# Kernel tuning notes

Hardware: AMD Instinct MI355X
Metric: run time of the kernel (lower is better)

Reference implementation:

```python
import jax, jax.numpy as jnp
import numpy as np

N = 50000   # nodes
E = 800000  # edges
IN = 128    # in_channels
H = 256     # hidden_channels
G = 128     # graphs in batch
NEG_SLOPE = 0.2


def _gat_conv(x, src, dst, W, a_src, a_dst, b):
    # PyG GATConv, heads=1: xp = W x; e_ij = LeakyReLU(a_src.xp_j + a_dst.xp_i);
    # softmax over incoming edges of target i; out_i = sum_j alpha_ij xp_j + b
    xp = x @ W                                   # [N, H]
    e = jax.nn.leaky_relu(xp[src] @ a_src + xp[dst] @ a_dst, NEG_SLOPE)  # [Et]
    m = jax.ops.segment_max(e, dst, num_segments=N)
    m = jnp.where(jnp.isfinite(m), m, 0.0)
    p = jnp.exp(e - m[dst])
    denom = jax.ops.segment_sum(p, dst, num_segments=N)
    alpha = p / denom[dst]
    return jax.ops.segment_sum(alpha[:, None] * xp[src], dst, num_segments=N) + b


def _gru_step_h0(x, W_ih, W_hh, b_ih, b_hh):
    # torch.nn.GRU, seq_len=1, h0=0. Gate order: r, z, n.
    gi = x @ W_ih.T + b_ih                       # [N, 3H]
    i_r, i_z, i_n = jnp.split(gi, 3, axis=-1)
    h_r, h_z, h_n = jnp.split(b_hh, 3)           # h0=0 -> hidden gates are biases
    r = jax.nn.sigmoid(i_r + h_r)
    z = jax.nn.sigmoid(i_z + h_z)
    n = jnp.tanh(i_n + r * h_n)
    return (1.0 - z) * n                         # + z * h0 (=0)


def setup_inputs() -> dict:
    key = jax.random.key(0)
    ks = jax.random.split(key, 18)
    s = 0.05
    inp = {
        "x": jax.random.normal(ks[0], (N, IN), jnp.float32),
        "edge_index": jax.random.randint(ks[1], (2, E), 0, N, dtype=jnp.int32).astype(jnp.int64),
        "batch": jnp.sort(jax.random.randint(ks[2], (N,), 0, G, dtype=jnp.int32)).astype(jnp.int64),
        # GAT layer 0 (in->H) and layer 1 (H->H)
        "W0": jax.random.normal(ks[3], (IN, H), jnp.float32) * s,
        "a_src0": jax.random.normal(ks[4], (H,), jnp.float32) * s,
        "a_dst0": jax.random.normal(ks[5], (H,), jnp.float32) * s,
        "b0": jnp.zeros((H,), jnp.float32),
        "W1": jax.random.normal(ks[6], (H, H), jnp.float32) * s,
        "a_src1": jax.random.normal(ks[7], (H,), jnp.float32) * s,
        "a_dst1": jax.random.normal(ks[8], (H,), jnp.float32) * s,
        "b1": jnp.zeros((H,), jnp.float32),
        # GRU(H, H)
        "W_ih": jax.random.normal(ks[9], (3 * H, H), jnp.float32) * s,
        "W_hh": jax.random.normal(ks[10], (3 * H, H), jnp.float32) * s,
        "b_ih": jnp.zeros((3 * H,), jnp.float32),
        "b_hh": jnp.zeros((3 * H,), jnp.float32),
        # super_node_fc
        "Wf": jax.random.normal(ks[11], (H, H), jnp.float32) * s,
        "bf": jnp.zeros((H,), jnp.float32),
    }
    return inp


def reference(x, edge_index, batch, W0, a_src0, a_dst0, b0, W1, a_src1, a_dst1, b1,
              W_ih, W_hh, b_ih, b_hh, Wf, bf):
    # add self loops (PyG GATConv default)
    loops = jnp.arange(N, dtype=edge_index.dtype)
    src = jnp.concatenate([edge_index[0], loops])
    dst = jnp.concatenate([edge_index[1], loops])

    h = jax.nn.relu(_gat_conv(x, src, dst, W0, a_src0, a_dst0, b0))  # dropout=identity (eval)
    h = jax.nn.relu(_gat_conv(h, src, dst, W1, a_src1, a_dst1, b1))

    h = _gru_step_h0(h, W_ih, W_hh, b_ih, b_hh)                      # [N, H]

    h = jax.ops.segment_sum(h, batch, num_segments=G)                # global_add_pool [G, H]
    super_node = jnp.mean(h, axis=0, keepdims=True)                  # [1, H]
    super_node = jax.nn.relu(super_node @ Wf.T + bf)
    return jnp.concatenate([h, jnp.broadcast_to(super_node, (G, H))], axis=1)  # [G, 2H]
```

## Files before the change

### kernel.cpp

```cpp
#include <hip/hip_runtime.h>
#include <hip/hip_fp16.h>
#include <math.h>

#define N_NODES 50000
#define N_PAD   50176
#define N_EDGES 800000
#define ET (N_EDGES + N_NODES)
#define IN_CH 128
#define H 256
#define G_GRAPHS 128
#define NEG_SLOPE 0.2f
#define GRU_CHUNK 25000
#define NB 391

typedef __attribute__((ext_vector_type(8))) short short8;
typedef __attribute__((ext_vector_type(4))) float f32x4;
typedef unsigned short u16;
typedef unsigned char u8;

#if __has_builtin(__builtin_amdgcn_cvt_f32_fp8) && __has_builtin(__builtin_amdgcn_cvt_pk_fp8_f32)
#define USE_FP8_BUILTINS 1
#else
#define USE_FP8_BUILTINS 0
#endif

__device__ inline u16 f2bf(float v) {
    unsigned u = __float_as_uint(v);
    unsigned r = (u + 0x7FFFu + ((u >> 16) & 1u)) >> 16;
    return (u16)r;
}
__device__ inline float bf2f(u16 v) {
    return __uint_as_float(((unsigned)v) << 16);
}

#if USE_FP8_BUILTINS
#define FP8_WSCALE 1.0f
__device__ inline unsigned fp8_pack4(float a, float b, float c, float d) {
    int v = 0;
    v = __builtin_amdgcn_cvt_pk_fp8_f32(a, b, v, false);
    v = __builtin_amdgcn_cvt_pk_fp8_f32(c, d, v, true);
    return (unsigned)v;
}
__device__ inline void fp8_dec4(unsigned rv, float& f0, float& f1, float& f2, float& f3) {
    f0 = __builtin_amdgcn_cvt_f32_fp8((int)rv, 0);
    f1 = __builtin_amdgcn_cvt_f32_fp8((int)rv, 1);
    f2 = __builtin_amdgcn_cvt_f32_fp8((int)rv, 2);
    f3 = __builtin_amdgcn_cvt_f32_fp8((int)rv, 3);
}
#else
#define FP8_WSCALE 256.0f
__device__ inline u8 fp8_enc1(float f) {
    unsigned u = __float_as_uint(f);
    unsigned s = (u >> 31) << 7;
    float a = fabsf(f);
    if (a >= 448.f) return (u8)(s | 0x7E);
    unsigned bits = __float_as_uint(a);
    int exp = (int)((bits >> 23) & 255) - 127;
    unsigned m23 = bits & 0x7fffff;
    if (exp < -6) {
        int m = (int)rintf(a * 512.f);
        if (m >= 8) return (u8)(s | (1 << 3));
        return (u8)(s | m);
    }
    int e8 = exp + 7;
    unsigned m = m23 >> 20, rem = m23 & 0xFFFFF;
    if (rem > 0x80000 || (rem == 0x80000 && (m & 1))) m++;
    if (m == 8) { m = 0; e8++; }
    if (e8 > 15 || (e8 == 15 && m == 7)) return (u8)(s | 0x7E);
    return (u8)(s | (e8 << 3) | m);
}
__device__ inline unsigned fp8_pack4(float a, float b, float c, float d) {
    return (unsigned)fp8_enc1(a) | ((unsigned)fp8_enc1(b) << 8) |
           ((unsigned)fp8_enc1(c) << 16) | ((unsigned)fp8_enc1(d) << 24);
}
__device__ inline void fp8_dec4(unsigned rv, float& f0, float& f1, float& f2, float& f3) {
    unsigned hA = ((rv & 0x00800080u) << 8) | ((rv & 0x007f007fu) << 7);
    unsigned rs = rv >> 8;
    unsigned hB = ((rs & 0x00800080u) << 8) | ((rs & 0x007f007fu) << 7);
    __half2 a = *(__half2*)&hA;
    __half2 b = *(__half2*)&hB;
    f0 = __low2float(a);  f2 = __high2float(a);
    f1 = __low2float(b);  f3 = __high2float(b);
}
#endif

__device__ inline void async_cp16(const u16* g, u16* l) {
    __builtin_amdgcn_global_load_lds(
        (const __attribute__((address_space(1))) unsigned int*)g,
        (__attribute__((address_space(3))) unsigned int*)l,
        16, 0, 0);
}


__global__ __launch_bounds__(256) void bucket_hist(const int* __restrict__ ei,
                                                   int* __restrict__ gcnt) {
    __shared__ int h[NB];
    int t = threadIdx.x;
    for (int b = t; b < NB; b += 256) h[b] = 0;
    __syncthreads();
    for (int e = blockIdx.x * 256 + t; e < N_EDGES; e += gridDim.x * 256)
        atomicAdd(&h[ei[N_EDGES + e] >> 7], 1);
    __syncthreads();
    for (int b = t; b < NB; b += 256)
        if (h[b]) atomicAdd(&gcnt[b], h[b]);
}

__global__ __launch_bounds__(512) void bucket_scan(const int* __restrict__ gcnt,
                                                   int* __restrict__ off,
                                                   int* __restrict__ cur) {
    __shared__ int s[NB + 1];
    int t = threadIdx.x;
    if (t < NB) s[t] = gcnt[t];
    __syncthreads();
    if (t == 0) {
        int a = 0;
        for (int b = 0; b < NB; b++) { int c = s[b]; s[b] = a; a += c; }
        s[NB] = a;
    }
    __syncthreads();
    if (t <= NB) { off[t] = s[t]; if (t < NB) cur[t] = s[t]; }
}

#define EPT 16
__global__ __launch_bounds__(256) void bucket_scatter(const int* __restrict__ ei,
                                                      int* __restrict__ bucketCur,
                                                      int2* __restrict__ rec) {
    __shared__ int cnt[NB];
    __shared__ int base[NB];
    int t = threadIdx.x;
    for (int b = t; b < NB; b += 256) cnt[b] = 0;
    __syncthreads();
    int e0 = blockIdx.x * (256 * EPT);
    int sa[EPT], da[EPT], rk[EPT];
#pragma unroll
    for (int k = 0; k < EPT; k++) {
        int e = e0 + k * 256 + t;
        if (e < N_EDGES) {
            sa[k] = ei[e];
            da[k] = ei[N_EDGES + e];
            rk[k] = atomicAdd(&cnt[da[k] >> 7], 1);
        }
    }
    __syncthreads();
    for (int b = t; b < NB; b += 256) {
        int c = cnt[b];
        base[b] = c ? atomicAdd(&bucketCur[b], c) : 0;
    }
    __syncthreads();
#pragma unroll
    for (int k = 0; k < EPT; k++) {
        int e = e0 + k * 256 + t;
        if (e < N_EDGES) rec[base[da[k] >> 7] + rk[k]] = make_int2(sa[k], da[k]);
    }
}

__global__ __launch_bounds__(256) void node_hist(const int2* __restrict__ rec,
                                                 const int* __restrict__ off,
                                                 int* __restrict__ counts) {
    __shared__ int cnt[128];
    int b = blockIdx.x, t = threadIdx.x;
    if (t < 128) cnt[t] = 1;
    __syncthreads();
    int lo = off[b], hi = off[b + 1];
    for (int i = lo + t; i < hi; i += 256) atomicAdd(&cnt[rec[i].y & 127], 1);
    __syncthreads();
    int node = b * 128 + t;
    if (t < 128 && node < N_NODES) counts[node] = cnt[t];
}

__global__ __launch_bounds__(256) void scan_block(const int* __restrict__ in,
                                                  int* __restrict__ incl,
                                                  int* __restrict__ blockSums) {
    __shared__ int s[256];
    int t = threadIdx.x;
    int i = blockIdx.x * 256 + t;
    int v = (i < N_NODES) ? in[i] : 0;
    s[t] = v;
    __syncthreads();
    for (int off = 1; off < 256; off <<= 1) {
        int x = 0;
        if (t >= off) x = s[t - off];
        __syncthreads();
        if (t >= off) s[t] += x;
        __syncthreads();
    }
    if (i < N_NODES) incl[i] = s[t];
    if (t == 255) blockSums[blockIdx.x] = s[255];
}

__global__ __launch_bounds__(256) void scan_sums(const int* __restrict__ blockSums,
                                                 int* __restrict__ blockOff, int nb) {
    __shared__ int s[256];
    int t = threadIdx.x;
    int v = (t < nb) ? blockSums[t] : 0;
    s[t] = v;
    __syncthreads();
    for (int off = 1; off < 256; off <<= 1) {
        int x = 0;
        if (t >= off) x = s[t - off];
        __syncthreads();
        if (t >= off) s[t] += x;
        __syncthreads();
    }
    if (t < nb) blockOff[t] = s[t] - v;
}

__global__ __launch_bounds__(256) void scan_finalize(const int* __restrict__ incl,
                                                     const int* __restrict__ blockOff,
                                                     int* __restrict__ indptr) {
    int i = blockIdx.x * 256 + threadIdx.x;
    if (i < N_NODES) indptr[i + 1] = incl[i] + blockOff[i >> 8];
    if (i == 0) indptr[0] = 0;
}

__global__ __launch_bounds__(256) void final_scatter(const int2* __restrict__ rec,
                                                     const int* __restrict__ off,
                                                     const int* __restrict__ indptr,
                                                     int* __restrict__ eidsSrc) {
    __shared__ int cur[128];
    int b = blockIdx.x, t = threadIdx.x;
    int node = b * 128 + t;
    if (t < 128 && node < N_NODES) {
        int ip = indptr[node];
        eidsSrc[ip] = node;
        cur[t] = ip + 1;
    }
    __syncthreads();
    int lo = off[b], hi = off[b + 1];
    for (int i = lo + t; i < hi; i += 256) {
        int2 r = rec[i];
        int pos = atomicAdd(&cur[r.y & 127], 1);
        eidsSrc[pos] = r.x;
    }
}

__global__ __launch_bounds__(256) void prep_kernel(const float* __restrict__ x,
                                                   const float* __restrict__ Wih,
                                                   const float* __restrict__ W0,
                                                   const float* __restrict__ W1,
                                                   u16* __restrict__ x_bf,
                                                   u16* __restrict__ Wih_bf,
                                                   u16* __restrict__ W0t,
                                                   u16* __restrict__ W1t) {
    int i = blockIdx.x * 256 + threadIdx.x;
    int seg = blockIdx.y;
    if (seg == 0) {
        if (i < N_NODES * IN_CH / 4) {
            float4 v = *(const float4*)&x[i * 4];
            ushort4 o = {f2bf(v.x), f2bf(v.y), f2bf(v.z), f2bf(v.w)};
            *(ushort4*)&x_bf[i * 4] = o;
        }
    } else if (seg == 1) {
        if (i < 3 * H * H / 4) {
            float4 v = *(const float4*)&Wih[i * 4];
            ushort4 o = {f2bf(v.x), f2bf(v.y), f2bf(v.z), f2bf(v.w)};
            *(ushort4*)&Wih_bf[i * 4] = o;
        }
    } else if (seg == 2) {
        if (i < IN_CH * H) {
            int k = i / H, n = i % H;
            W0t[(size_t)n * IN_CH + k] = f2bf(W0[i]);
        }
    } else {
        if (i < H * H) {
            int k = i / H, n = i % H;
            W1t[(size_t)n * H + k] = f2bf(W1[i]);
        }
    }
}

__global__ __launch_bounds__(256, 2) void gemm_wide(const u16* __restrict__ A,
                                                    const u16* __restrict__ Bt,
                                                    u16* __restrict__ C,
                                                    int M, int K, int Ntot) {
    __shared__ u16 As[128][32];
    __shared__ u16 Bs[256][32];
    int t = threadIdx.x;
    int m0 = blockIdx.x * 128;
    int n0 = blockIdx.y * 256;
    int wave = t >> 6, lane = t & 63;
    int wm = (wave >> 1) * 64, wn = (wave & 1) * 128;
    int lrow = lane & 15;
    int lq = lane >> 4;

    f32x4 acc[4][8];
#pragma unroll
    for (int i = 0; i < 4; i++)
#pragma unroll
        for (int j = 0; j < 8; j++)
            acc[i][j] = (f32x4){0.f, 0.f, 0.f, 0.f};

    int r0 = t >> 2, q0 = t & 3;
    const u16* gA0 = A + (size_t)(m0 + r0) * K + q0 * 8;
    const u16* gA1 = gA0 + (size_t)64 * K;
    const u16* gB0 = Bt + (size_t)(n0 + r0) * K + q0 * 8;
    const u16* gB1 = gB0 + (size_t)64 * K;
    const u16* gB2 = gB0 + (size_t)128 * K;
    const u16* gB3 = gB0 + (size_t)192 * K;
    u16* lA0 = &As[0][0] + t * 8;
    u16* lA1 = lA0 + 256 * 8;
    u16* lB0 = &Bs[0][0] + t * 8;
    u16* lB1 = lB0 + 256 * 8;
    u16* lB2 = lB0 + 512 * 8;
    u16* lB3 = lB0 + 768 * 8;

    for (int k0 = 0; k0 < K; k0 += 32) {
        __syncthreads();
        async_cp16(gA0 + k0, lA0);
        async_cp16(gA1 + k0, lA1);
        async_cp16(gB0 + k0, lB0);
        async_cp16(gB1 + k0, lB1);
        async_cp16(gB2 + k0, lB2);
        async_cp16(gB3 + k0, lB3);
        __syncthreads();
        short8 af[4], bfr[8];
#pragma unroll
        for (int i = 0; i < 4; i++)
            af[i] = *(const short8*)&As[wm + i * 16 + lrow][lq * 8];
#pragma unroll
        for (int j = 0; j < 8; j++)
            bfr[j] = *(const short8*)&Bs[wn + j * 16 + lrow][lq * 8];
#pragma unroll
        for (int i = 0; i < 4; i++)
#pragma unroll
            for (int j = 0; j < 8; j++)
                acc[i][j] = __builtin_amdgcn_mfma_f32_16x16x32_bf16(af[i], bfr[j], acc[i][j], 0, 0, 0);
    }
#pragma unroll
    for (int i = 0; i < 4; i++) {
#pragma unroll
        for (int reg = 0; reg < 4; reg++) {
            int gm = m0 + wm + i * 16 + lq * 4 + reg;
            if (gm < M) {
#pragma unroll
                for (int j = 0; j < 8; j++) {
                    int gn = n0 + wn + j * 16 + lrow;
                    C[(size_t)gm * Ntot + gn] = f2bf(acc[i][j][reg]);
                }
            }
        }
    }
}

__global__ __launch_bounds__(256) void sdot_fp8(const u16* __restrict__ xp,
                                                const float* __restrict__ a_src,
                                                const float* __restrict__ a_dst,
                                                float* __restrict__ s_src,
                                                float* __restrict__ s_dst,
                                                u8* __restrict__ xp8) {
    int wave = threadIdx.x >> 6, lane = threadIdx.x & 63;
    int n = blockIdx.x * 4 + wave;
    int col = lane << 2;
    ushort4 v = *(const ushort4*)&xp[(size_t)n * H + col];
    float4 a1 = *(const float4*)&a_src[col];
    float4 a2 = *(const float4*)&a_dst[col];
    float x0 = bf2f(v.x), x1 = bf2f(v.y), x2 = bf2f(v.z), x3 = bf2f(v.w);
    *(unsigned*)&xp8[(size_t)n * H + col] = fp8_pack4(x0, x1, x2, x3);
    float d1 = x0 * a1.x + x1 * a1.y + x2 * a1.z + x3 * a1.w;
    float d2 = x0 * a2.x + x1 * a2.y + x2 * a2.z + x3 * a2.w;
#pragma unroll
    for (int off = 32; off; off >>= 1) {
        d1 += __shfl_xor(d1, off);
        d2 += __shfl_xor(d2, off);
    }
    if (lane == 0) { s_src[n] = d1; s_dst[n] = d2; }
}

__global__ __launch_bounds__(256) void gat_agg_fp8(const u8* __restrict__ xp8,
                                                   const float* __restrict__ s_src,
                                                   const float* __restrict__ s_dst,
                                                   const int* __restrict__ indptr,
                                                   const int* __restrict__ eidsSrc,
                                                   const float* __restrict__ bias,
                                                   u16* __restrict__ out) {
    __shared__ int   sS[4][64];
    __shared__ float sW[4][64];
    int wave = threadIdx.x >> 6, lane = threadIdx.x & 63;
    int n = blockIdx.x * 4 + wave;
    int start = indptr[n];
    int deg = indptr[n + 1] - start;
    float sdn = s_dst[n];
    int col = lane << 2;
    float a0 = 0.f, a1 = 0.f, a2 = 0.f, a3 = 0.f;

    if (deg <= 64) {
        int s = 0;
        float v = -1e30f;
        if (lane < deg) {
            s = eidsSrc[start + lane];
            float u = s_src[s] + sdn;
            v = (u >= 0.f) ? u : NEG_SLOPE * u;
        }
        float m = v;
#pragma unroll
        for (int off = 32; off; off >>= 1) m = fmaxf(m, __shfl_xor(m, off));
        float pw = (lane < deg) ? expf(v - m) : 0.f;
        float dsum = pw;
#pragma unroll
        for (int off = 32; off; off >>= 1) dsum += __shfl_xor(dsum, off);
        sS[wave][lane] = s;
        sW[wave][lane] = pw * (FP8_WSCALE / dsum);
        int j = 0;
        for (; j + 8 <= deg; j += 8) {
            unsigned rv[8];
            float wv[8];
#pragma unroll
            for (int k = 0; k < 8; k++) {
                int sj = sS[wave][j + k];
                wv[k] = sW[wave][j + k];
                rv[k] = *(const unsigned*)&xp8[(size_t)sj * H + col];
            }
#pragma unroll
            for (int k = 0; k < 8; k++) {
                float f0, f1, f2, f3;
                fp8_dec4(rv[k], f0, f1, f2, f3);
                a0 += wv[k] * f0; a1 += wv[k] * f1;
                a2 += wv[k] * f2; a3 += wv[k] * f3;
            }
        }
        for (; j < deg; j++) {
            int sj = sS[wave][j];
            float wj = sW[wave][j];
            unsigned rv = *(const unsigned*)&xp8[(size_t)sj * H + col];
            float f0, f1, f2, f3;
            fp8_dec4(rv, f0, f1, f2, f3);
            a0 += wj * f0; a1 += wj * f1; a2 += wj * f2; a3 += wj * f3;
        }
    } else {
        float m = -1e30f;
        for (int i = lane; i < deg; i += 64) {
            int s = eidsSrc[start + i];
            float u = s_src[s] + sdn;
            u = (u >= 0.f) ? u : NEG_SLOPE * u;
            m = fmaxf(m, u);
        }
#pragma unroll
        for (int off = 32; off; off >>= 1) m = fmaxf(m, __shfl_xor(m, off));
        float dsum = 0.f;
        for (int i = lane; i < deg; i += 64) {
            int s = eidsSrc[start + i];
            float u = s_src[s] + sdn;
            u = (u >= 0.f) ? u : NEG_SLOPE * u;
            dsum += expf(u - m);
        }
#pragma unroll
        for (int off = 32; off; off >>= 1) dsum += __shfl_xor(dsum, off);
        float dinv = FP8_WSCALE / dsum;
        for (int base = 0; base < deg; base += 64) {
            int cnt = min(64, deg - base);
            int s = 0; float w = 0.f;
            if (lane < cnt) {
                s = eidsSrc[start + base + lane];
                float u = s_src[s] + sdn;
                u = (u >= 0.f) ? u : NEG_SLOPE * u;
                w = expf(u - m) * dinv;
            }
            sS[wave][lane] = s;
            sW[wave][lane] = w;
            for (int j = 0; j < cnt; j++) {
                int sj = sS[wave][j];
                float wj = sW[wave][j];
                unsigned rv = *(const unsigned*)&xp8[(size_t)sj * H + col];
                float f0, f1, f2, f3;
                fp8_dec4(rv, f0, f1, f2, f3);
                a0 += wj * f0; a1 += wj * f1; a2 += wj * f2; a3 += wj * f3;
            }
        }
    }
    float4 bv = *(const float4*)&bias[col];
    ushort4 o;
    o.x = f2bf(fmaxf(a0 + bv.x, 0.f));
    o.y = f2bf(fmaxf(a1 + bv.y, 0.f));
    o.z = f2bf(fmaxf(a2 + bv.z, 0.f));
    o.w = f2bf(fmaxf(a3 + bv.w, 0.f));
    *(ushort4*)&out[(size_t)n * H + col] = o;
}

__global__ __launch_bounds__(256) void gru_gates_pool(const u16* __restrict__ gates,
                                                      const float* __restrict__ b_ih,
                                                      const float* __restrict__ b_hh,
                                                      const int* __restrict__ batch,
                                                      float* __restrict__ pooled,
                                                      int nodeBase, int nodeCount) {
    int t = threadIdx.x;
    int i0 = blockIdx.x * 16;
    if (i0 >= nodeCount) return;
    float bir = b_ih[t], biz = b_ih[256 + t], bin_ = b_ih[512 + t];
    float bhr = b_hh[t], bhz = b_hh[256 + t], bhn = b_hh[512 + t];
    int iend = min(16, nodeCount - i0);
    float acc = 0.f;
    int cur_g = batch[nodeBase + i0];
    for (int i = 0; i < iend; i++) {
        size_t row = (size_t)(i0 + i) * 768;
        float ir = bf2f(gates[row + t]);
        float iz = bf2f(gates[row + 256 + t]);
        float in_ = bf2f(gates[row + 512 + t]);
        float r = 1.f / (1.f + expf(-(ir + bir + bhr)));
        float z = 1.f / (1.f + expf(-(iz + biz + bhz)));
        float nn = tanhf(in_ + bin_ + r * bhn);
        float h = (1.f - z) * nn;
        int g = batch[nodeBase + i0 + i];
        if (g != cur_g) {
            atomicAdd(&pooled[(size_t)cur_g * H + t], acc);
            acc = 0.f;
            cur_g = g;
        }
        acc += h;
    }
    atomicAdd(&pooled[(size_t)cur_g * H + t], acc);
}

__global__ __launch_bounds__(256) void super_kernel(const float* __restrict__ pooled,
                                                    const float* __restrict__ Wf,
                                                    const float* __restrict__ bf,
                                                    float* __restrict__ sup) {
    __shared__ float smean[256];
    int t = threadIdx.x;
    float s = 0.f;
    for (int g = 0; g < G_GRAPHS; g++) s += pooled[(size_t)g * H + t];
    smean[t] = s / (float)G_GRAPHS;
    __syncthreads();
    float acc = 0.f;
    for (int k = 0; k < H; k++) acc += smean[k] * Wf[(size_t)t * H + k];
    acc += bf[t];
    sup[t] = fmaxf(acc, 0.f);
}

__global__ __launch_bounds__(256) void writeout(const float* __restrict__ pooled,
                                                const float* __restrict__ sup,
                                                float* __restrict__ out) {
    int idx = blockIdx.x * 256 + threadIdx.x;
    int g = idx >> 9, c = idx & 511;
    out[idx] = (c < H) ? pooled[(size_t)g * H + c] : sup[c - H];
}

extern "C" void kernel_launch(void* const* d_in, const int* in_sizes, int n_in,
                              void* d_out, int out_size, void* d_ws, size_t ws_size,
                              hipStream_t stream) {
    const float* x      = (const float*)d_in[0];
    const int*   ei     = (const int*)d_in[1];
    const int*   batch  = (const int*)d_in[2];
    const float* W0     = (const float*)d_in[3];
    const float* a_src0 = (const float*)d_in[4];
    const float* a_dst0 = (const float*)d_in[5];
    const float* b0     = (const float*)d_in[6];
    const float* W1     = (const float*)d_in[7];
    const float* a_src1 = (const float*)d_in[8];
    const float* a_dst1 = (const float*)d_in[9];
    const float* b1     = (const float*)d_in[10];
    const float* W_ih   = (const float*)d_in[11];
    const float* b_ih   = (const float*)d_in[13];
    const float* b_hh   = (const float*)d_in[14];
    const float* Wf     = (const float*)d_in[15];
    const float* bf     = (const float*)d_in[16];
    float* out = (float*)d_out;

    char* p = (char*)d_ws;
    auto alloc = [&](size_t bytes) -> void* {
        void* r = (void*)p;
        p += (bytes + 255) & ~(size_t)255;
        return r;
    };
    u16*   xp_bf  = (u16*)alloc((size_t)N_PAD * H * 2);
    u16*   h_bf   = (u16*)alloc((size_t)N_PAD * H * 2);
    u16*   x_bf   = (u16*)alloc((size_t)N_PAD * IN_CH * 2);
    u8*    xp8    = (u8*)x_bf;
    u16*   gatesC = (u16*)alloc((size_t)GRU_CHUNK * 3 * H * 2);
    u16*   W0t    = (u16*)alloc((size_t)H * IN_CH * 2);
    u16*   W1t    = (u16*)alloc((size_t)H * H * 2);
    u16*   Wih_bf = (u16*)alloc((size_t)3 * H * H * 2);
    float* s_src  = (float*)alloc((size_t)N_NODES * 4);
    float* s_dst  = (float*)alloc((size_t)N_NODES * 4);
    int2*  rec    = (int2*)alloc((size_t)N_EDGES * 8);
    int*   eidsSrc= (int*)alloc((size_t)ET * 4);
    int*   counts = (int*)alloc((size_t)N_NODES * 4);
    int*   incl   = (int*)alloc((size_t)N_NODES * 4);
    int*   indptr = (int*)alloc((size_t)(N_NODES + 1) * 4);
    int*   gBkt   = (int*)alloc((size_t)(NB + 1) * 4);
    int*   bktOff = (int*)alloc((size_t)(NB + 1) * 4);
    int*   bktCur = (int*)alloc((size_t)(NB + 1) * 4);
    int*   bSums  = (int*)alloc(256 * 4);
    int*   bOff   = (int*)alloc(256 * 4);
    float* pooled = (float*)alloc((size_t)G_GRAPHS * H * 4);
    float* sup    = (float*)alloc((size_t)H * 4);

    const int SB = (N_NODES + 255) / 256;
    hipMemsetAsync(gBkt, 0, (size_t)NB * 4, stream);
    bucket_hist<<<NB, 256, 0, stream>>>(ei, gBkt);
    bucket_scan<<<1, 512, 0, stream>>>(gBkt, bktOff, bktCur);
    bucket_scatter<<<(N_EDGES + 256 * EPT - 1) / (256 * EPT), 256, 0, stream>>>(ei, bktCur, rec);
    node_hist<<<NB, 256, 0, stream>>>(rec, bktOff, counts);
    scan_block<<<SB, 256, 0, stream>>>(counts, incl, bSums);
    scan_sums<<<1, 256, 0, stream>>>(bSums, bOff, SB);
    scan_finalize<<<SB, 256, 0, stream>>>(incl, bOff, indptr);
    final_scatter<<<NB, 256, 0, stream>>>(rec, bktOff, indptr, eidsSrc);

    prep_kernel<<<dim3((N_NODES * IN_CH / 4 + 255) / 256, 4), 256, 0, stream>>>(
        x, W_ih, W0, W1, x_bf, Wih_bf, W0t, W1t);

    const int MB = (N_NODES + 127) / 128;
    const int WB = N_NODES / 4;
    gemm_wide<<<dim3(MB, 1), 256, 0, stream>>>(x_bf, W0t, xp_bf, N_NODES, IN_CH, H);
    sdot_fp8<<<WB, 256, 0, stream>>>(xp_bf, a_src0, a_dst0, s_src, s_dst, xp8);
    gat_agg_fp8<<<WB, 256, 0, stream>>>(xp8, s_src, s_dst, indptr, eidsSrc, b0, h_bf);
    gemm_wide<<<dim3(MB, 1), 256, 0, stream>>>(h_bf, W1t, xp_bf, N_NODES, H, H);
    sdot_fp8<<<WB, 256, 0, stream>>>(xp_bf, a_src1, a_dst1, s_src, s_dst, xp8);
    gat_agg_fp8<<<WB, 256, 0, stream>>>(xp8, s_src, s_dst, indptr, eidsSrc, b1, h_bf);
    hipMemsetAsync(pooled, 0, (size_t)G_GRAPHS * H * 4, stream);
    for (int base = 0; base < N_NODES; base += GRU_CHUNK) {
        int cnt = min(GRU_CHUNK, N_NODES - base);
        gemm_wide<<<dim3((cnt + 127) / 128, 3), 256, 0, stream>>>(
            h_bf + (size_t)base * H, Wih_bf, gatesC, cnt, H, 3 * H);
        gru_gates_pool<<<(cnt + 15) / 16, 256, 0, stream>>>(gatesC, b_ih, b_hh, batch, pooled, base, cnt);
    }
    super_kernel<<<1, 256, 0, stream>>>(pooled, Wf, bf, sup);
    writeout<<<(G_GRAPHS * 2 * H) / 256, 256, 0, stream>>>(pooled, sup, out);
}
```

Before: 394.6 us.

## Fuse attention dot products and FP8 encode into GEMM epilogue; merge CSR build kernels

The GAT projection GEMM now computes the per-node source and destination attention scores and writes FP8 features directly in its epilogue through a shared-memory staging buffer. This removes the separate sdot pass and the bf16 round trip of xp. The four CSR-building kernels (node histogram, two-level scan, finalize, scatter) collapse into one per-bucket kernel that does a local scan, using bucket offsets plus 128 self-loops per bucket as the base. Smaller edits pack src/weight into int2 in LDS for aggregation and use packed FP8 decode when it is available. The fused epilogue adds LDS traffic and register pressure to the GEMM, and the rows it writes are not bounds-guarded, so they land in the padded buffer.

```diff
diff --git a/kernel.cpp b/kernel.cpp
--- a/kernel.cpp
+++ b/kernel.cpp
@@ -15,6 +15,7 @@
 
 typedef __attribute__((ext_vector_type(8))) short short8;
 typedef __attribute__((ext_vector_type(4))) float f32x4;
+typedef __attribute__((ext_vector_type(2))) float f32x2;
 typedef unsigned short u16;
 typedef unsigned char u8;
 
@@ -23,6 +24,11 @@
 #else
 #define USE_FP8_BUILTINS 0
 #endif
+#if USE_FP8_BUILTINS && __has_builtin(__builtin_amdgcn_cvt_pk_f32_fp8)
+#define HAVE_PK_DEC 1
+#else
+#define HAVE_PK_DEC 0
+#endif
 
 __device__ inline u16 f2bf(float v) {
     unsigned u = __float_as_uint(v);
@@ -35,21 +41,25 @@
 
 #if USE_FP8_BUILTINS
 #define FP8_WSCALE 1.0f
-__device__ inline unsigned fp8_pack4(float a, float b, float c, float d) {
-    int v = 0;
-    v = __builtin_amdgcn_cvt_pk_fp8_f32(a, b, v, false);
-    v = __builtin_amdgcn_cvt_pk_fp8_f32(c, d, v, true);
-    return (unsigned)v;
+__device__ inline u8 fp8_enc(float v) {
+    int r = __builtin_amdgcn_cvt_pk_fp8_f32(v, v, 0, false);
+    return (u8)(r & 0xFF);
 }
 __device__ inline void fp8_dec4(unsigned rv, float& f0, float& f1, float& f2, float& f3) {
+#if HAVE_PK_DEC
+    f32x2 lo = __builtin_amdgcn_cvt_pk_f32_fp8((int)rv, false);
+    f32x2 hi = __builtin_amdgcn_cvt_pk_f32_fp8((int)rv, true);
+    f0 = lo.x; f1 = lo.y; f2 = hi.x; f3 = hi.y;
+#else
     f0 = __builtin_amdgcn_cvt_f32_fp8((int)rv, 0);
     f1 = __builtin_amdgcn_cvt_f32_fp8((int)rv, 1);
     f2 = __builtin_amdgcn_cvt_f32_fp8((int)rv, 2);
     f3 = __builtin_amdgcn_cvt_f32_fp8((int)rv, 3);
+#endif
 }
 #else
 #define FP8_WSCALE 256.0f
-__device__ inline u8 fp8_enc1(float f) {
+__device__ inline u8 fp8_enc(float f) {
     unsigned u = __float_as_uint(f);
     unsigned s = (u >> 31) << 7;
     float a = fabsf(f);
@@ -69,10 +79,6 @@
     if (e8 > 15 || (e8 == 15 && m == 7)) return (u8)(s | 0x7E);
     return (u8)(s | (e8 << 3) | m);
 }
-__device__ inline unsigned fp8_pack4(float a, float b, float c, float d) {
-    return (unsigned)fp8_enc1(a) | ((unsigned)fp8_enc1(b) << 8) |
-           ((unsigned)fp8_enc1(c) << 16) | ((unsigned)fp8_enc1(d) << 24);
-}
 __device__ inline void fp8_dec4(unsigned rv, float& f0, float& f1, float& f2, float& f3) {
     unsigned hA = ((rv & 0x00800080u) << 8) | ((rv & 0x007f007fu) << 7);
     unsigned rs = rv >> 8;
@@ -91,7 +97,6 @@
         16, 0, 0);
 }
 
-
 __global__ __launch_bounds__(256) void bucket_hist(const int* __restrict__ ei,
                                                    int* __restrict__ gcnt) {
     __shared__ int h[NB];
@@ -154,79 +159,40 @@
     }
 }
 
-__global__ __launch_bounds__(256) void node_hist(const int2* __restrict__ rec,
+__global__ __launch_bounds__(256) void build_csr(const int2* __restrict__ rec,
                                                  const int* __restrict__ off,
-                                                 int* __restrict__ counts) {
+                                                 int* __restrict__ indptr,
+                                                 int* __restrict__ eidsSrc) {
     __shared__ int cnt[128];
+    __shared__ int scn[128];
+    __shared__ int cur[128];
     int b = blockIdx.x, t = threadIdx.x;
-    if (t < 128) cnt[t] = 1;
+    int nInB = N_NODES - b * 128;
+    if (nInB > 128) nInB = 128;
+    if (t < 128) cnt[t] = 0;
     __syncthreads();
     int lo = off[b], hi = off[b + 1];
     for (int i = lo + t; i < hi; i += 256) atomicAdd(&cnt[rec[i].y & 127], 1);
     __syncthreads();
-    int node = b * 128 + t;
-    if (t < 128 && node < N_NODES) counts[node] = cnt[t];
-}
-
-__global__ __launch_bounds__(256) void scan_block(const int* __restrict__ in,
-                                                  int* __restrict__ incl,
-                                                  int* __restrict__ blockSums) {
-    __shared__ int s[256];
-    int t = threadIdx.x;
-    int i = blockIdx.x * 256 + t;
-    int v = (i < N_NODES) ? in[i] : 0;
-    s[t] = v;
-    __syncthreads();
-    for (int off = 1; off < 256; off <<= 1) {
-        int x = 0;
-        if (t >= off) x = s[t - off];
+    if (t < 128) scn[t] = cnt[t] + 1;
+    __syncthreads();
+    for (int o = 1; o < 128; o <<= 1) {
+        int v = 0;
+        if (t < 128 && t >= o) v = scn[t - o];
         __syncthreads();
-        if (t >= off) s[t] += x;
+        if (t < 128 && t >= o) scn[t] += v;
         __syncthreads();
     }
-    if (i < N_NODES) incl[i] = s[t];
-    if (t == 255) blockSums[blockIdx.x] = s[255];
-}
-
-__global__ __launch_bounds__(256) void scan_sums(const int* __restrict__ blockSums,
-                                                 int* __restrict__ blockOff, int nb) {
-    __shared__ int s[256];
-    int t = threadIdx.x;
-    int v = (t < nb) ? blockSums[t] : 0;
-    s[t] = v;
-    __syncthreads();
-    for (int off = 1; off < 256; off <<= 1) {
-        int x = 0;
-        if (t >= off) x = s[t - off];
-        __syncthreads();
-        if (t >= off) s[t] += x;
-        __syncthreads();
-    }
-    if (t < nb) blockOff[t] = s[t] - v;
-}
-
-__global__ __launch_bounds__(256) void scan_finalize(const int* __restrict__ incl,
-                                                     const int* __restrict__ blockOff,
-                                                     int* __restrict__ indptr) {
-    int i = blockIdx.x * 256 + threadIdx.x;
-    if (i < N_NODES) indptr[i + 1] = incl[i] + blockOff[i >> 8];
-    if (i == 0) indptr[0] = 0;
-}
-
-__global__ __launch_bounds__(256) void final_scatter(const int2* __restrict__ rec,
-                                                     const int* __restrict__ off,
-                                                     const int* __restrict__ indptr,
-                                                     int* __restrict__ eidsSrc) {
-    __shared__ int cur[128];
-    int b = blockIdx.x, t = threadIdx.x;
-    int node = b * 128 + t;
-    if (t < 128 && node < N_NODES) {
-        int ip = indptr[node];
-        eidsSrc[ip] = node;
-        cur[t] = ip + 1;
-    }
-    __syncthreads();
-    int lo = off[b], hi = off[b + 1];
+    int base = off[b] + 128 * b;
+    if (t < nInB) {
+        int start = base + (t ? scn[t - 1] : 0);
+        int node = b * 128 + t;
+        indptr[node] = start;
+        eidsSrc[start] = node;
+        cur[t] = start + 1;
+    }
+    if (b == 0 && t == 0) indptr[N_NODES] = ET;
+    __syncthreads();
     for (int i = lo + t; i < hi; i += 256) {
         int2 r = rec[i];
         int pos = atomicAdd(&cur[r.y & 127], 1);
@@ -269,12 +235,21 @@
     }
 }
 
+struct StageMem { u16 As[128][32]; u16 Bs[256][32]; };
+struct EpiMem   { u8 xt[128][256]; float rS[4][64]; float rD[4][64]; };
+union ShMem     { StageMem s; EpiMem e; };
+
+template <bool FUSE>
 __global__ __launch_bounds__(256, 2) void gemm_wide(const u16* __restrict__ A,
                                                     const u16* __restrict__ Bt,
                                                     u16* __restrict__ C,
+                                                    u8* __restrict__ C8,
+                                                    const float* __restrict__ avS,
+                                                    const float* __restrict__ avD,
+                                                    float* __restrict__ sS,
+                                                    float* __restrict__ sD,
                                                     int M, int K, int Ntot) {
-    __shared__ u16 As[128][32];
-    __shared__ u16 Bs[256][32];
+    __shared__ ShMem shm;
     int t = threadIdx.x;
     int m0 = blockIdx.x * 128;
     int n0 = blockIdx.y * 256;
@@ -297,9 +272,9 @@
     const u16* gB1 = gB0 + (size_t)64 * K;
     const u16* gB2 = gB0 + (size_t)128 * K;
     const u16* gB3 = gB0 + (size_t)192 * K;
-    u16* lA0 = &As[0][0] + t * 8;
+    u16* lA0 = &shm.s.As[0][0] + t * 8;
     u16* lA1 = lA0 + 256 * 8;
-    u16* lB0 = &Bs[0][0] + t * 8;
+    u16* lB0 = &shm.s.Bs[0][0] + t * 8;
     u16* lB1 = lB0 + 256 * 8;
     u16* lB2 = lB0 + 512 * 8;
     u16* lB3 = lB0 + 768 * 8;
@@ -316,54 +291,83 @@
         short8 af[4], bfr[8];
 #pragma unroll
         for (int i = 0; i < 4; i++)
-            af[i] = *(const short8*)&As[wm + i * 16 + lrow][lq * 8];
+            af[i] = *(const short8*)&shm.s.As[wm + i * 16 + lrow][lq * 8];
 #pragma unroll
         for (int j = 0; j < 8; j++)
-            bfr[j] = *(const short8*)&Bs[wn + j * 16 + lrow][lq * 8];
+            bfr[j] = *(const short8*)&shm.s.Bs[wn + j * 16 + lrow][lq * 8];
 #pragma unroll
         for (int i = 0; i < 4; i++)
 #pragma unroll
             for (int j = 0; j < 8; j++)
                 acc[i][j] = __builtin_amdgcn_mfma_f32_16x16x32_bf16(af[i], bfr[j], acc[i][j], 0, 0, 0);
     }
-#pragma unroll
-    for (int i = 0; i < 4; i++) {
-#pragma unroll
-        for (int reg = 0; reg < 4; reg++) {
-            int gm = m0 + wm + i * 16 + lq * 4 + reg;
-            if (gm < M) {
+
+    if constexpr (FUSE) {
+        __syncthreads();
+        float aS[8], aD[8];
+#pragma unroll
+        for (int j = 0; j < 8; j++) {
+            aS[j] = avS[wn + j * 16 + lrow];
+            aD[j] = avD[wn + j * 16 + lrow];
+        }
+#pragma unroll
+        for (int i = 0; i < 4; i++) {
+#pragma unroll
+            for (int reg = 0; reg < 4; reg++) {
+                float ps = 0.f, pd = 0.f;
+                int rloc = wm + i * 16 + lq * 4 + reg;
 #pragma unroll
                 for (int j = 0; j < 8; j++) {
-                    int gn = n0 + wn + j * 16 + lrow;
-                    C[(size_t)gm * Ntot + gn] = f2bf(acc[i][j][reg]);
+                    float v = acc[i][j][reg];
+                    ps += v * aS[j];
+                    pd += v * aD[j];
+                    shm.e.xt[rloc][wn + j * 16 + lrow] = fp8_enc(v);
+                }
+#pragma unroll
+                for (int m = 1; m < 16; m <<= 1) {
+                    ps += __shfl_xor(ps, m);
+                    pd += __shfl_xor(pd, m);
+                }
+                if (lrow == 0) {
+                    shm.e.rS[wave][i * 16 + lq * 4 + reg] = ps;
+                    shm.e.rD[wave][i * 16 + lq * 4 + reg] = pd;
                 }
             }
         }
-    }
-}
-
-__global__ __launch_bounds__(256) void sdot_fp8(const u16* __restrict__ xp,
-                                                const float* __restrict__ a_src,
-                                                const float* __restrict__ a_dst,
-                                                float* __restrict__ s_src,
-                                                float* __restrict__ s_dst,
-                                                u8* __restrict__ xp8) {
-    int wave = threadIdx.x >> 6, lane = threadIdx.x & 63;
-    int n = blockIdx.x * 4 + wave;
-    int col = lane << 2;
-    ushort4 v = *(const ushort4*)&xp[(size_t)n * H + col];
-    float4 a1 = *(const float4*)&a_src[col];
-    float4 a2 = *(const float4*)&a_dst[col];
-    float x0 = bf2f(v.x), x1 = bf2f(v.y), x2 = bf2f(v.z), x3 = bf2f(v.w);
-    *(unsigned*)&xp8[(size_t)n * H + col] = fp8_pack4(x0, x1, x2, x3);
-    float d1 = x0 * a1.x + x1 * a1.y + x2 * a1.z + x3 * a1.w;
-    float d2 = x0 * a2.x + x1 * a2.y + x2 * a2.z + x3 * a2.w;
-#pragma unroll
-    for (int off = 32; off; off >>= 1) {
-        d1 += __shfl_xor(d1, off);
-        d2 += __shfl_xor(d2, off);
-    }
-    if (lane == 0) { s_src[n] = d1; s_dst[n] = d2; }
+        __syncthreads();
+        if (t < 128) {
+            int w0 = (t >> 6) << 1;
+            int l = t & 63;
+            int gm = m0 + t;
+            if (gm < M) {
+                sS[gm] = shm.e.rS[w0][l] + shm.e.rS[w0 + 1][l];
+                sD[gm] = shm.e.rD[w0][l] + shm.e.rD[w0 + 1][l];
+            }
+        }
+#pragma unroll
+        for (int pass = 0; pass < 8; pass++) {
+            int idx = pass * 256 + t;
+            int row = idx >> 4;
+            int c16 = (idx & 15) << 4;
+            int4 vv = *(const int4*)&shm.e.xt[row][c16];
+            *(int4*)&C8[(size_t)(m0 + row) * 256 + c16] = vv;
+        }
+    } else {
+#pragma unroll
+        for (int i = 0; i < 4; i++) {
+#pragma unroll
+            for (int reg = 0; reg < 4; reg++) {
+                int gm = m0 + wm + i * 16 + lq * 4 + reg;
+                if (gm < M) {
+#pragma unroll
+                    for (int j = 0; j < 8; j++) {
+                        int gn = n0 + wn + j * 16 + lrow;
+                        C[(size_t)gm * Ntot + gn] = f2bf(acc[i][j][reg]);
+                    }
+                }
+            }
+        }
+    }
 }
 
 __global__ __launch_bounds__(256) void gat_agg_fp8(const u8* __restrict__ xp8,
@@ -373,8 +377,7 @@
                                                    const int* __restrict__ eidsSrc,
                                                    const float* __restrict__ bias,
                                                    u16* __restrict__ out) {
-    __shared__ int   sS[4][64];
-    __shared__ float sW[4][64];
+    __shared__ int2 sSW[4][64];
     int wave = threadIdx.x >> 6, lane = threadIdx.x & 63;
     int n = blockIdx.x * 4 + wave;
     int start = indptr[n];
@@ -398,17 +401,17 @@
         float dsum = pw;
 #pragma unroll
         for (int off = 32; off; off >>= 1) dsum += __shfl_xor(dsum, off);
-        sS[wave][lane] = s;
-        sW[wave][lane] = pw * (FP8_WSCALE / dsum);
+        float w = pw * (FP8_WSCALE / dsum);
+        sSW[wave][lane] = make_int2(s, __float_as_int(w));
         int j = 0;
         for (; j + 8 <= deg; j += 8) {
             unsigned rv[8];
             float wv[8];
 #pragma unroll
             for (int k = 0; k < 8; k++) {
-                int sj = sS[wave][j + k];
-                wv[k] = sW[wave][j + k];
-                rv[k] = *(const unsigned*)&xp8[(size_t)sj * H + col];
+                int2 sw = sSW[wave][j + k];
+                wv[k] = __int_as_float(sw.y);
+                rv[k] = *(const unsigned*)&xp8[(size_t)sw.x * H + col];
             }
 #pragma unroll
             for (int k = 0; k < 8; k++) {
@@ -419,9 +422,9 @@
             }
         }
         for (; j < deg; j++) {
-            int sj = sS[wave][j];
-            float wj = sW[wave][j];
-            unsigned rv = *(const unsigned*)&xp8[(size_t)sj * H + col];
+            int2 sw = sSW[wave][j];
+            float wj = __int_as_float(sw.y);
+            unsigned rv = *(const unsigned*)&xp8[(size_t)sw.x * H + col];
             float f0, f1, f2, f3;
             fp8_dec4(rv, f0, f1, f2, f3);
             a0 += wj * f0; a1 += wj * f1; a2 += wj * f2; a3 += wj * f3;
@@ -455,12 +458,11 @@
                 u = (u >= 0.f) ? u : NEG_SLOPE * u;
                 w = expf(u - m) * dinv;
             }
-            sS[wave][lane] = s;
-            sW[wave][lane] = w;
+            sSW[wave][lane] = make_int2(s, __float_as_int(w));
             for (int j = 0; j < cnt; j++) {
-                int sj = sS[wave][j];
-                float wj = sW[wave][j];
-                unsigned rv = *(const unsigned*)&xp8[(size_t)sj * H + col];
+                int2 sw = sSW[wave][j];
+                float wj = __int_as_float(sw.y);
+                unsigned rv = *(const unsigned*)&xp8[(size_t)sw.x * H + col];
                 float f0, f1, f2, f3;
                 fp8_dec4(rv, f0, f1, f2, f3);
                 a0 += wj * f0; a1 += wj * f1; a2 += wj * f2; a3 += wj * f3;
@@ -561,10 +563,9 @@
         p += (bytes + 255) & ~(size_t)255;
         return r;
     };
-    u16*   xp_bf  = (u16*)alloc((size_t)N_PAD * H * 2);
     u16*   h_bf   = (u16*)alloc((size_t)N_PAD * H * 2);
     u16*   x_bf   = (u16*)alloc((size_t)N_PAD * IN_CH * 2);
-    u8*    xp8    = (u8*)x_bf;
+    u8*    xp8    = (u8*)alloc((size_t)N_PAD * H);
     u16*   gatesC = (u16*)alloc((size_t)GRU_CHUNK * 3 * H * 2);
     u16*   W0t    = (u16*)alloc((size_t)H * IN_CH * 2);
     u16*   W1t    = (u16*)alloc((size_t)H * H * 2);
@@ -573,44 +574,36 @@
     float* s_dst  = (float*)alloc((size_t)N_NODES * 4);
     int2*  rec    = (int2*)alloc((size_t)N_EDGES * 8);
     int*   eidsSrc= (int*)alloc((size_t)ET * 4);
-    int*   counts = (int*)alloc((size_t)N_NODES * 4);
-    int*   incl   = (int*)alloc((size_t)N_NODES * 4);
     int*   indptr = (int*)alloc((size_t)(N_NODES + 1) * 4);
     int*   gBkt   = (int*)alloc((size_t)(NB + 1) * 4);
     int*   bktOff = (int*)alloc((size_t)(NB + 1) * 4);
     int*   bktCur = (int*)alloc((size_t)(NB + 1) * 4);
-    int*   bSums  = (int*)alloc(256 * 4);
-    int*   bOff   = (int*)alloc(256 * 4);
     float* pooled = (float*)alloc((size_t)G_GRAPHS * H * 4);
     float* sup    = (float*)alloc((size_t)H * 4);
 
-    const int SB = (N_NODES + 255) / 256;
     hipMemsetAsync(gBkt, 0, (size_t)NB * 4, stream);
     bucket_hist<<<NB, 256, 0, stream>>>(ei, gBkt);
     bucket_scan<<<1, 512, 0, stream>>>(gBkt, bktOff, bktCur);
     bucket_scatter<<<(N_EDGES + 256 * EPT - 1) / (256 * EPT), 256, 0, stream>>>(ei, bktCur, rec);
-    node_hist<<<NB, 256, 0, stream>>>(rec, bktOff, counts);
-    scan_block<<<SB, 256, 0, stream>>>(counts, incl, bSums);
-    scan_sums<<<1, 256, 0, stream>>>(bSums, bOff, SB);
-    scan_finalize<<<SB, 256, 0, stream>>>(incl, bOff, indptr);
-    final_scatter<<<NB, 256, 0, stream>>>(rec, bktOff, indptr, eidsSrc);
+    build_csr<<<NB, 256, 0, stream>>>(rec, bktOff, indptr, eidsSrc);
 
     prep_kernel<<<dim3((N_NODES * IN_CH / 4 + 255) / 256, 4), 256, 0, stream>>>(
         x, W_ih, W0, W1, x_bf, Wih_bf, W0t, W1t);
 
     const int MB = (N_NODES + 127) / 128;
     const int WB = N_NODES / 4;
-    gemm_wide<<<dim3(MB, 1), 256, 0, stream>>>(x_bf, W0t, xp_bf, N_NODES, IN_CH, H);
-    sdot_fp8<<<WB, 256, 0, stream>>>(xp_bf, a_src0, a_dst0, s_src, s_dst, xp8);
+    gemm_wide<true><<<dim3(MB, 1), 256, 0, stream>>>(
+        x_bf, W0t, nullptr, xp8, a_src0, a_dst0, s_src, s_dst, N_NODES, IN_CH, H);
     gat_agg_fp8<<<WB, 256, 0, stream>>>(xp8, s_src, s_dst, indptr, eidsSrc, b0, h_bf);
-    gemm_wide<<<dim3(MB, 1), 256, 0, stream>>>(h_bf, W1t, xp_bf, N_NODES, H, H);
-    sdot_fp8<<<WB, 256, 0, stream>>>(xp_bf, a_src1, a_dst1, s_src, s_dst, xp8);
+    gemm_wide<true><<<dim3(MB, 1), 256, 0, stream>>>(
+        h_bf, W1t, nullptr, xp8, a_src1, a_dst1, s_src, s_dst, N_NODES, H, H);
     gat_agg_fp8<<<WB, 256, 0, stream>>>(xp8, s_src, s_dst, indptr, eidsSrc, b1, h_bf);
     hipMemsetAsync(pooled, 0, (size_t)G_GRAPHS * H * 4, stream);
     for (int base = 0; base < N_NODES; base += GRU_CHUNK) {
         int cnt = min(GRU_CHUNK, N_NODES - base);
-        gemm_wide<<<dim3((cnt + 127) / 128, 3), 256, 0, stream>>>(
-            h_bf + (size_t)base * H, Wih_bf, gatesC, cnt, H, 3 * H);
+        gemm_wide<false><<<dim3((cnt + 127) / 128, 3), 256, 0, stream>>>(
+            h_bf + (size_t)base * H, Wih_bf, gatesC, nullptr, nullptr, nullptr, nullptr, nullptr,
+            cnt, H, 3 * H);
         gru_gates_pool<<<(cnt + 15) / 16, 256, 0, stream>>>(gatesC, b_ih, b_hh, batch, pooled, base, cnt);
     }
     super_kernel<<<1, 256, 0, stream>>>(pooled, Wf, bf, sup);
```

Result: slower. 422.0 us (+6.9%).
